# Kernel optimization log

Hardware: AMD Instinct MI355X
Metric: run time of the kernel (lower is better)

Reference implementation:

```python
import jax, jax.numpy as jnp
import numpy as np

N_NODES = 1_000_000
N_EDGES = 16_000_000
N_FEAT = 128
NUM_GRAPHS = 8192


def setup_inputs() -> dict:
    key = jax.random.key(0)
    k_x, k_e, k_b, k_w, k_pw, k_pb = jax.random.split(key, 6)
    x = jax.random.normal(k_x, (N_NODES, N_FEAT), dtype=jnp.float32)
    edge_index = jax.random.randint(k_e, (2, N_EDGES), 0, N_NODES, dtype=jnp.int64)
    batch = jnp.sort(jax.random.randint(k_b, (N_NODES,), 0, NUM_GRAPHS, dtype=jnp.int64))
    # GCNConv lin weight (F -> 1, no bias), xavier-ish scale
    W = jax.random.normal(k_w, (N_FEAT, 1), dtype=jnp.float32) * (6.0 / (N_FEAT + 1)) ** 0.5
    # post_pool Linear(1, 1, bias=True)
    pp_w = jax.random.normal(k_pw, (1, 1), dtype=jnp.float32)
    pp_b = jax.random.normal(k_pb, (1,), dtype=jnp.float32) * 0.1
    return {"x": x, "W": W, "pp_w": pp_w, "pp_b": pp_b,
            "edge_index": edge_index, "batch": batch}


def reference(x, W, pp_w, pp_b, edge_index, batch):
    N = x.shape[0]
    h = x @ W  # [N, 1] — tiny feature after GCNConv projection
    # add self-loops (PyG GCNConv default)
    loops = jnp.arange(N, dtype=edge_index.dtype)
    src = jnp.concatenate([edge_index[0], loops])  # message sources (col j)
    dst = jnp.concatenate([edge_index[1], loops])  # aggregation targets (row i)
    # symmetric degree normalization: deg over targets incl. self-loops
    deg = jax.ops.segment_sum(jnp.ones(src.shape[0], dtype=h.dtype), dst,
                              num_segments=N)
    dinv = jnp.where(deg > 0, jax.lax.rsqrt(deg), 0.0)
    norm = dinv[src] * dinv[dst]  # [E+N]
    # gather -> normalize -> scatter-add
    agg = jax.ops.segment_sum(norm[:, None] * h[src], dst, num_segments=N)  # [N,1]
    # global_add_pool by graph id
    pooled = jax.ops.segment_sum(agg, batch, num_segments=NUM_GRAPHS)  # [G,1]
    return pooled @ pp_w.T + pp_b  # Linear(1,1)
```

## Files before the change

kernel.cpp:

```cpp
#include <hip/hip_runtime.h>
#include <hip/hip_fp16.h>

#define NUM_GRAPHS 8192
#define BSHIFT 12
#define BSIZE 4096
#define CHUNK 8192

__global__ void __launch_bounds__(256)
pair_scatter_kernel(const int* __restrict__ src, const int* __restrict__ dst,
                    int E, int nchunks, int NBUK, int cap,
                    unsigned* __restrict__ cursor, unsigned* __restrict__ slab) {
    __shared__ unsigned cnt[256];
    __shared__ unsigned lbase[256];
    __shared__ unsigned sbase[256];
    __shared__ unsigned staged[CHUNK];
    __shared__ unsigned char sbuck[CHUNK];
    __shared__ unsigned s_tot;

    const int4* s4 = (const int4*)src;
    const int4* d4 = (const int4*)dst;
    int E4 = E >> 2;
    int tid = threadIdx.x;

    for (int chunk = blockIdx.x; chunk < nchunks; chunk += gridDim.x) {
        cnt[tid] = 0; __syncthreads();
        int b4 = chunk * (CHUNK / 4);
        int4 vd[8], vs[8];
        unsigned short r[32];
        #pragma unroll
        for (int k = 0; k < 8; ++k) {
            int idx = b4 + k * 256 + tid;
            if (idx < E4) { vd[k] = d4[idx]; vs[k] = s4[idx]; }
            else          { vd[k] = make_int4(-1, -1, -1, -1); }
        }
        #pragma unroll
        for (int k = 0; k < 8; ++k) {
            if (vd[k].x >= 0) {
                r[4*k+0] = (unsigned short)atomicAdd(&cnt[vd[k].x >> BSHIFT], 1u);
                r[4*k+1] = (unsigned short)atomicAdd(&cnt[vd[k].y >> BSHIFT], 1u);
                r[4*k+2] = (unsigned short)atomicAdd(&cnt[vd[k].z >> BSHIFT], 1u);
                r[4*k+3] = (unsigned short)atomicAdd(&cnt[vd[k].w >> BSHIFT], 1u);
            }
        }
        __syncthreads();
        lbase[tid] = cnt[tid]; __syncthreads();
        #pragma unroll
        for (int off = 1; off < 256; off <<= 1) {
            unsigned a = (tid >= off) ? lbase[tid - off] : 0u;
            __syncthreads();
            lbase[tid] += a;
            __syncthreads();
        }
        if (tid == 255) s_tot = lbase[255];
        if (tid < NBUK && cnt[tid]) sbase[tid] = atomicAdd(&cursor[tid], cnt[tid]);
        unsigned excl = lbase[tid] - cnt[tid];
        __syncthreads();
        lbase[tid] = excl;
        __syncthreads();

        #pragma unroll
        for (int k = 0; k < 8; ++k) {
            if (vd[k].x >= 0) {
                int d0 = vd[k].x, d1 = vd[k].y, d2 = vd[k].z, d3 = vd[k].w;
                unsigned b0 = (unsigned)d0 >> BSHIFT, b1 = (unsigned)d1 >> BSHIFT;
                unsigned b2 = (unsigned)d2 >> BSHIFT, b3 = (unsigned)d3 >> BSHIFT;
                unsigned p0 = lbase[b0] + r[4*k+0];
                unsigned p1 = lbase[b1] + r[4*k+1];
                unsigned p2 = lbase[b2] + r[4*k+2];
                unsigned p3 = lbase[b3] + r[4*k+3];
                staged[p0] = ((unsigned)(d0 & (BSIZE - 1)) << 20) | (unsigned)vs[k].x;
                staged[p1] = ((unsigned)(d1 & (BSIZE - 1)) << 20) | (unsigned)vs[k].y;
                staged[p2] = ((unsigned)(d2 & (BSIZE - 1)) << 20) | (unsigned)vs[k].z;
                staged[p3] = ((unsigned)(d3 & (BSIZE - 1)) << 20) | (unsigned)vs[k].w;
                sbuck[p0] = (unsigned char)b0;
                sbuck[p1] = (unsigned char)b1;
                sbuck[p2] = (unsigned char)b2;
                sbuck[p3] = (unsigned char)b3;
            }
        }
        __syncthreads();

        unsigned tot = s_tot;
        for (unsigned pos = tid; pos < tot; pos += 256) {
            unsigned b = sbuck[pos];
            unsigned gp = sbase[b] + (pos - lbase[b]);
            if (gp < (unsigned)cap) slab[(size_t)b * cap + gp] = staged[pos];
        }
        __syncthreads();
    }
    if (blockIdx.x == 0 && tid < (E & 3)) {
        int i = (E & ~3) + tid;
        int d = dst[i];
        unsigned p = atomicAdd(&cursor[d >> BSHIFT], 1u);
        if (p < (unsigned)cap)
            slab[(size_t)(d >> BSHIFT) * cap + p] =
                ((unsigned)(d & (BSIZE - 1)) << 20) | (unsigned)src[i];
    }
}

__global__ void __launch_bounds__(1024)
slab_hist_kernel(const unsigned* __restrict__ slab, int cap,
                 const unsigned* __restrict__ cursor,
                 unsigned* __restrict__ deg, int N) {
    __shared__ unsigned hist[BSIZE];
    int b = blockIdx.x, tid = threadIdx.x;
    unsigned n = cursor[b]; if (n > (unsigned)cap) n = cap;
    for (int t = tid; t < BSIZE; t += 1024) hist[t] = 0;
    __syncthreads();
    const unsigned* s = slab + (size_t)b * cap;
    for (unsigned i = tid; i < n; i += 1024) atomicAdd(&hist[s[i] >> 20], 1u);
    __syncthreads();
    int base = b << BSHIFT;
    int lim = N - base; if (lim > BSIZE) lim = BSIZE;
    for (int t = tid; t < lim; t += 1024) deg[base + t] = hist[t];
}

__global__ void node_kernel(const float* __restrict__ x,
                            const float* __restrict__ W,
                            const unsigned* __restrict__ deg,
                            const int* __restrict__ batch,
                            unsigned short* __restrict__ hsh,
                            unsigned* __restrict__ pkw, int N) {
    int gtid = blockIdx.x * blockDim.x + threadIdx.x;
    int wave = gtid >> 6;
    int lane = threadIdx.x & 63;
    int half = lane >> 5;
    int l32  = lane & 31;
    int node = wave * 2 + half;
    if (node >= N) return;

    const float4* xr = (const float4*)(x + (size_t)node * 128);
    float4 xv = xr[l32];
    float4 wv = ((const float4*)W)[l32];
    float v = xv.x * wv.x + xv.y * wv.y + xv.z * wv.z + xv.w * wv.w;
    #pragma unroll
    for (int d = 16; d >= 1; d >>= 1) v += __shfl_xor(v, d);

    if (l32 == 0) {
        float di = rsqrtf((float)(deg[node] + 1u));
        hsh[node] = __half_as_ushort(__float2half(di * v));
        pkw[node] = ((unsigned)batch[node] << 16) | __half_as_ushort(__float2half(di));
    }
}

__global__ void __launch_bounds__(1024)
aggregate_kernel(const unsigned* __restrict__ slab, int cap,
                 const unsigned* __restrict__ cursor,
                 const unsigned* __restrict__ pkw,
                 const unsigned short* __restrict__ hsh,
                 float* __restrict__ pooled, int N) {
    __shared__ float pool[NUM_GRAPHS];
    __shared__ unsigned pkw_s[BSIZE];
    int b = blockIdx.x, tid = threadIdx.x;
    int base = b << BSHIFT;
    int lim = N - base; if (lim > BSIZE) lim = BSIZE;

    for (int t = tid; t < NUM_GRAPHS; t += 1024) pool[t] = 0.0f;
    for (int t = tid; t < BSIZE; t += 1024) pkw_s[t] = (t < lim) ? pkw[base + t] : 0u;
    __syncthreads();

    for (int t = tid; t < lim; t += 1024) {
        unsigned w = pkw_s[t];
        float di = __half2float(__ushort_as_half((unsigned short)(w & 0xFFFFu)));
        float c = di * __half2float(__ushort_as_half(hsh[base + t]));
        atomicAdd(&pool[w >> 16], c);
    }

    unsigned n = cursor[b]; if (n > (unsigned)cap) n = cap;
    const unsigned* s = slab + (size_t)b * cap;
    for (unsigned i = tid; i < n; i += 1024) {
        unsigned e = s[i];
        unsigned w = pkw_s[e >> 20];
        float hv = __half2float(__ushort_as_half(hsh[e & 0xFFFFFu]));
        float di = __half2float(__ushort_as_half((unsigned short)(w & 0xFFFFu)));
        atomicAdd(&pool[w >> 16], hv * di);
    }
    __syncthreads();

    int g_lo = (int)(pkw_s[0] >> 16);
    int g_hi = (lim > 0) ? (int)(pkw_s[lim - 1] >> 16) : g_lo;
    for (int g = g_lo + tid; g <= g_hi; g += 1024) atomicAdd(&pooled[g], pool[g]);
}

__global__ void out_kernel(const float* __restrict__ pooled,
                           const float* __restrict__ pp_w,
                           const float* __restrict__ pp_b,
                           float* __restrict__ out) {
    int g = blockIdx.x * blockDim.x + threadIdx.x;
    if (g < NUM_GRAPHS) out[g] = pooled[g] * pp_w[0] + pp_b[0];
}

__global__ void deg_atomic_kernel(const int* __restrict__ dst, int E,
                                  unsigned* __restrict__ deg) {
    int tid = blockIdx.x * blockDim.x + threadIdx.x;
    int stride = gridDim.x * blockDim.x;
    for (int i = tid; i < E; i += stride) atomicAdd(&deg[dst[i]], 1u);
}

__global__ void pool_self_fb_kernel(const unsigned short* __restrict__ hsh,
                                    const unsigned* __restrict__ pkw,
                                    float* __restrict__ pooled, int N) {
    int i = blockIdx.x * blockDim.x + threadIdx.x;
    if (i >= N) return;
    unsigned w = pkw[i];
    float di = __half2float(__ushort_as_half((unsigned short)(w & 0xFFFFu)));
    atomicAdd(&pooled[w >> 16], di * __half2float(__ushort_as_half(hsh[i])));
}

__global__ void __launch_bounds__(512)
edge_direct_kernel(const int* __restrict__ src, const int* __restrict__ dst, int E,
                   const unsigned short* __restrict__ hsh,
                   const unsigned* __restrict__ pkw,
                   float* __restrict__ pooled) {
    __shared__ float pool[NUM_GRAPHS];
    for (int g = threadIdx.x; g < NUM_GRAPHS; g += 512) pool[g] = 0.0f;
    __syncthreads();
    int tid = blockIdx.x * 512 + threadIdx.x;
    int stride = gridDim.x * 512;
    for (int i = tid; i < E; i += stride) {
        unsigned w = pkw[dst[i]];
        float c = __half2float(__ushort_as_half(hsh[src[i]])) *
                  __half2float(__ushort_as_half((unsigned short)(w & 0xFFFFu)));
        atomicAdd(&pool[w >> 16], c);
    }
    __syncthreads();
    for (int g = threadIdx.x; g < NUM_GRAPHS; g += 512)
        if (pool[g] != 0.0f) atomicAdd(&pooled[g], pool[g]);
}

extern "C" void kernel_launch(void* const* d_in, const int* in_sizes, int n_in,
                              void* d_out, int out_size, void* d_ws, size_t ws_size,
                              hipStream_t stream) {
    const float* x    = (const float*)d_in[0];
    const float* W    = (const float*)d_in[1];
    const float* pp_w = (const float*)d_in[2];
    const float* pp_b = (const float*)d_in[3];
    const int*   ei   = (const int*)d_in[4];
    const int*   batch= (const int*)d_in[5];
    float* out = (float*)d_out;

    const int E = in_sizes[4] / 2;
    const int N = in_sizes[5];
    const int* src = ei;
    const int* dst = ei + E;
    int NBUK = (N + BSIZE - 1) >> BSHIFT;

    char* ws = (char*)d_ws;
    size_t off = 0;
    auto alloc = [&](size_t bytes) {
        size_t o = off; off = (off + bytes + 255) & ~(size_t)255; return o;
    };
    size_t deg_off    = alloc((size_t)N * 4);
    size_t hsh_off    = alloc((size_t)N * 2);
    size_t pkw_off    = alloc((size_t)N * 4);
    size_t pooled_off = alloc((size_t)NUM_GRAPHS * 4);
    size_t cursor_off = alloc(1024);

    int cap = E / NBUK + E / NBUK / 8 + 2048;
    size_t slab_off = alloc((size_t)NBUK * (size_t)cap * 4);

    bool slab_ok = (NBUK <= 256) && (N <= (1 << 20)) && (off <= ws_size);

    unsigned*       deg    = (unsigned*)(ws + deg_off);
    unsigned short* hsh    = (unsigned short*)(ws + hsh_off);
    unsigned*       pkw    = (unsigned*)(ws + pkw_off);
    float*          pooled = (float*)(ws + pooled_off);
    unsigned*       cursor = (unsigned*)(ws + cursor_off);
    unsigned*       slab   = (unsigned*)(ws + slab_off);

    hipMemsetAsync(pooled, 0, (size_t)NUM_GRAPHS * 4, stream);

    if (slab_ok) {
        hipMemsetAsync(cursor, 0, 1024, stream);
        int E4 = E >> 2;
        int nchunks = (E4 + (CHUNK / 4 - 1)) / (CHUNK / 4);
        int grid = nchunks < 2048 ? nchunks : 2048;
        pair_scatter_kernel<<<grid, 256, 0, stream>>>(src, dst, E, nchunks, NBUK,
                                                      cap, cursor, slab);
        slab_hist_kernel<<<NBUK, 1024, 0, stream>>>(slab, cap, cursor, deg, N);

        int node_blocks = (N + 7) / 8;
        node_kernel<<<node_blocks, 256, 0, stream>>>(x, W, deg, batch, hsh, pkw, N);

        aggregate_kernel<<<NBUK, 1024, 0, stream>>>(slab, cap, cursor, pkw, hsh,
                                                    pooled, N);
    } else {
        hipMemsetAsync(deg, 0, (size_t)N * 4, stream);
        deg_atomic_kernel<<<2048, 256, 0, stream>>>(dst, E, deg);
        int node_blocks = (N + 7) / 8;
        node_kernel<<<node_blocks, 256, 0, stream>>>(x, W, deg, batch, hsh, pkw, N);
        pool_self_fb_kernel<<<(N + 255) / 256, 256, 0, stream>>>(hsh, pkw, pooled, N);
        edge_direct_kernel<<<512, 512, 0, stream>>>(src, dst, E, hsh, pkw, pooled);
    }

    out_kernel<<<(NUM_GRAPHS + 255) / 256, 256, 0, stream>>>(pooled, pp_w, pp_b, out);
}
```

Before: 325.9 us.

## Run x@W projection concurrently with edge scatter via heterogeneous block roles

The edge bucket-scatter kernel and the node projection (x@W) now share one launch. One in three blocks does the scatter and the other two compute h, so the bandwidth-heavy 512MB read of x overlaps with the edge pass. The deg-to-normalisation step moves into the histogram kernel, which writes hsh/pkw directly and removes the separate node kernel and the deg buffer round trip. This adds an fp32 h buffer and makes the scatter's grid size fixed, so the two roles can contend for bandwidth and finish unevenly.

```diff
diff --git a/kernel.cpp b/kernel.cpp
--- a/kernel.cpp
+++ b/kernel.cpp
@@ -5,11 +5,15 @@
 #define BSHIFT 12
 #define BSIZE 4096
 #define CHUNK 8192
+#define SBLOCKS 1024
+#define HBLOCKS 2048
 
 __global__ void __launch_bounds__(256)
-pair_scatter_kernel(const int* __restrict__ src, const int* __restrict__ dst,
-                    int E, int nchunks, int NBUK, int cap,
-                    unsigned* __restrict__ cursor, unsigned* __restrict__ slab) {
+fused_scatter_h_kernel(const int* __restrict__ src, const int* __restrict__ dst,
+                       int E, int nchunks, int NBUK, int cap,
+                       unsigned* __restrict__ cursor, unsigned* __restrict__ slab,
+                       const float* __restrict__ x, const float* __restrict__ W,
+                       float* __restrict__ h, int N) {
     __shared__ unsigned cnt[256];
     __shared__ unsigned lbase[256];
     __shared__ unsigned sbase[256];
@@ -17,91 +21,115 @@
     __shared__ unsigned char sbuck[CHUNK];
     __shared__ unsigned s_tot;
 
-    const int4* s4 = (const int4*)src;
-    const int4* d4 = (const int4*)dst;
-    int E4 = E >> 2;
+    int bid = blockIdx.x;
+    int rem = bid % 3;
+    int grp = bid / 3;
     int tid = threadIdx.x;
 
-    for (int chunk = blockIdx.x; chunk < nchunks; chunk += gridDim.x) {
-        cnt[tid] = 0; __syncthreads();
-        int b4 = chunk * (CHUNK / 4);
-        int4 vd[8], vs[8];
-        unsigned short r[32];
-        #pragma unroll
-        for (int k = 0; k < 8; ++k) {
-            int idx = b4 + k * 256 + tid;
-            if (idx < E4) { vd[k] = d4[idx]; vs[k] = s4[idx]; }
-            else          { vd[k] = make_int4(-1, -1, -1, -1); }
+    if (rem == 0) {
+        const int4* s4 = (const int4*)src;
+        const int4* d4 = (const int4*)dst;
+        int E4 = E >> 2;
+        for (int chunk = grp; chunk < nchunks; chunk += SBLOCKS) {
+            cnt[tid] = 0; __syncthreads();
+            int b4 = chunk * (CHUNK / 4);
+            int4 vd[8], vs[8];
+            unsigned short r[32];
+            #pragma unroll
+            for (int k = 0; k < 8; ++k) {
+                int idx = b4 + k * 256 + tid;
+                if (idx < E4) { vd[k] = d4[idx]; vs[k] = s4[idx]; }
+                else          { vd[k] = make_int4(-1, -1, -1, -1); }
+            }
+            #pragma unroll
+            for (int k = 0; k < 8; ++k) {
+                if (vd[k].x >= 0) {
+                    r[4*k+0] = (unsigned short)atomicAdd(&cnt[vd[k].x >> BSHIFT], 1u);
+                    r[4*k+1] = (unsigned short)atomicAdd(&cnt[vd[k].y >> BSHIFT], 1u);
+                    r[4*k+2] = (unsigned short)atomicAdd(&cnt[vd[k].z >> BSHIFT], 1u);
+                    r[4*k+3] = (unsigned short)atomicAdd(&cnt[vd[k].w >> BSHIFT], 1u);
+                }
+            }
+            __syncthreads();
+            lbase[tid] = cnt[tid]; __syncthreads();
+            #pragma unroll
+            for (int off = 1; off < 256; off <<= 1) {
+                unsigned a = (tid >= off) ? lbase[tid - off] : 0u;
+                __syncthreads();
+                lbase[tid] += a;
+                __syncthreads();
+            }
+            if (tid == 255) s_tot = lbase[255];
+            if (tid < NBUK && cnt[tid]) sbase[tid] = atomicAdd(&cursor[tid], cnt[tid]);
+            unsigned excl = lbase[tid] - cnt[tid];
+            __syncthreads();
+            lbase[tid] = excl;
+            __syncthreads();
+
+            #pragma unroll
+            for (int k = 0; k < 8; ++k) {
+                if (vd[k].x >= 0) {
+                    int d0 = vd[k].x, d1 = vd[k].y, d2 = vd[k].z, d3 = vd[k].w;
+                    unsigned b0 = (unsigned)d0 >> BSHIFT, b1 = (unsigned)d1 >> BSHIFT;
+                    unsigned b2 = (unsigned)d2 >> BSHIFT, b3 = (unsigned)d3 >> BSHIFT;
+                    unsigned p0 = lbase[b0] + r[4*k+0];
+                    unsigned p1 = lbase[b1] + r[4*k+1];
+                    unsigned p2 = lbase[b2] + r[4*k+2];
+                    unsigned p3 = lbase[b3] + r[4*k+3];
+                    staged[p0] = ((unsigned)(d0 & (BSIZE - 1)) << 20) | (unsigned)vs[k].x;
+                    staged[p1] = ((unsigned)(d1 & (BSIZE - 1)) << 20) | (unsigned)vs[k].y;
+                    staged[p2] = ((unsigned)(d2 & (BSIZE - 1)) << 20) | (unsigned)vs[k].z;
+                    staged[p3] = ((unsigned)(d3 & (BSIZE - 1)) << 20) | (unsigned)vs[k].w;
+                    sbuck[p0] = (unsigned char)b0;
+                    sbuck[p1] = (unsigned char)b1;
+                    sbuck[p2] = (unsigned char)b2;
+                    sbuck[p3] = (unsigned char)b3;
+                }
+            }
+            __syncthreads();
+
+            unsigned tot = s_tot;
+            for (unsigned pos = tid; pos < tot; pos += 256) {
+                unsigned b = sbuck[pos];
+                unsigned gp = sbase[b] + (pos - lbase[b]);
+                if (gp < (unsigned)cap) slab[(size_t)b * cap + gp] = staged[pos];
+            }
+            __syncthreads();
         }
-        #pragma unroll
-        for (int k = 0; k < 8; ++k) {
-            if (vd[k].x >= 0) {
-                r[4*k+0] = (unsigned short)atomicAdd(&cnt[vd[k].x >> BSHIFT], 1u);
-                r[4*k+1] = (unsigned short)atomicAdd(&cnt[vd[k].y >> BSHIFT], 1u);
-                r[4*k+2] = (unsigned short)atomicAdd(&cnt[vd[k].z >> BSHIFT], 1u);
-                r[4*k+3] = (unsigned short)atomicAdd(&cnt[vd[k].w >> BSHIFT], 1u);
-            }
+        if (grp == 0 && tid < (E & 3)) {
+            int i = (E & ~3) + tid;
+            int d = dst[i];
+            unsigned p = atomicAdd(&cursor[d >> BSHIFT], 1u);
+            if (p < (unsigned)cap)
+                slab[(size_t)(d >> BSHIFT) * cap + p] =
+                    ((unsigned)(d & (BSIZE - 1)) << 20) | (unsigned)src[i];
         }
-        __syncthreads();
-        lbase[tid] = cnt[tid]; __syncthreads();
-        #pragma unroll
-        for (int off = 1; off < 256; off <<= 1) {
-            unsigned a = (tid >= off) ? lbase[tid - off] : 0u;
-            __syncthreads();
-            lbase[tid] += a;
-            __syncthreads();
+    } else {
+        int hid = grp * 2 + (rem - 1);
+        int wave = tid >> 6;
+        int lane = tid & 63;
+        int half = lane >> 5;
+        int l32  = lane & 31;
+        float4 wv = ((const float4*)W)[l32];
+        for (int base = hid * 8; base < N; base += HBLOCKS * 8) {
+            int node = base + wave * 2 + half;
+            if (node < N) {
+                float4 xv = ((const float4*)(x + (size_t)node * 128))[l32];
+                float v = xv.x * wv.x + xv.y * wv.y + xv.z * wv.z + xv.w * wv.w;
+                #pragma unroll
+                for (int d = 16; d >= 1; d >>= 1) v += __shfl_xor(v, d);
+                if (l32 == 0) h[node] = v;
+            }
         }
-        if (tid == 255) s_tot = lbase[255];
-        if (tid < NBUK && cnt[tid]) sbase[tid] = atomicAdd(&cursor[tid], cnt[tid]);
-        unsigned excl = lbase[tid] - cnt[tid];
-        __syncthreads();
-        lbase[tid] = excl;
-        __syncthreads();
-
-        #pragma unroll
-        for (int k = 0; k < 8; ++k) {
-            if (vd[k].x >= 0) {
-                int d0 = vd[k].x, d1 = vd[k].y, d2 = vd[k].z, d3 = vd[k].w;
-                unsigned b0 = (unsigned)d0 >> BSHIFT, b1 = (unsigned)d1 >> BSHIFT;
-                unsigned b2 = (unsigned)d2 >> BSHIFT, b3 = (unsigned)d3 >> BSHIFT;
-                unsigned p0 = lbase[b0] + r[4*k+0];
-                unsigned p1 = lbase[b1] + r[4*k+1];
-                unsigned p2 = lbase[b2] + r[4*k+2];
-                unsigned p3 = lbase[b3] + r[4*k+3];
-                staged[p0] = ((unsigned)(d0 & (BSIZE - 1)) << 20) | (unsigned)vs[k].x;
-                staged[p1] = ((unsigned)(d1 & (BSIZE - 1)) << 20) | (unsigned)vs[k].y;
-                staged[p2] = ((unsigned)(d2 & (BSIZE - 1)) << 20) | (unsigned)vs[k].z;
-                staged[p3] = ((unsigned)(d3 & (BSIZE - 1)) << 20) | (unsigned)vs[k].w;
-                sbuck[p0] = (unsigned char)b0;
-                sbuck[p1] = (unsigned char)b1;
-                sbuck[p2] = (unsigned char)b2;
-                sbuck[p3] = (unsigned char)b3;
-            }
-        }
-        __syncthreads();
-
-        unsigned tot = s_tot;
-        for (unsigned pos = tid; pos < tot; pos += 256) {
-            unsigned b = sbuck[pos];
-            unsigned gp = sbase[b] + (pos - lbase[b]);
-            if (gp < (unsigned)cap) slab[(size_t)b * cap + gp] = staged[pos];
-        }
-        __syncthreads();
-    }
-    if (blockIdx.x == 0 && tid < (E & 3)) {
-        int i = (E & ~3) + tid;
-        int d = dst[i];
-        unsigned p = atomicAdd(&cursor[d >> BSHIFT], 1u);
-        if (p < (unsigned)cap)
-            slab[(size_t)(d >> BSHIFT) * cap + p] =
-                ((unsigned)(d & (BSIZE - 1)) << 20) | (unsigned)src[i];
     }
 }
 
 __global__ void __launch_bounds__(1024)
-slab_hist_kernel(const unsigned* __restrict__ slab, int cap,
-                 const unsigned* __restrict__ cursor,
-                 unsigned* __restrict__ deg, int N) {
+hist_finalize_kernel(const unsigned* __restrict__ slab, int cap,
+                     const unsigned* __restrict__ cursor,
+                     const float* __restrict__ h, const int* __restrict__ batch,
+                     unsigned short* __restrict__ hsh, unsigned* __restrict__ pkw,
+                     int N) {
     __shared__ unsigned hist[BSIZE];
     int b = blockIdx.x, tid = threadIdx.x;
     unsigned n = cursor[b]; if (n > (unsigned)cap) n = cap;
@@ -112,34 +140,11 @@
     __syncthreads();
     int base = b << BSHIFT;
     int lim = N - base; if (lim > BSIZE) lim = BSIZE;
-    for (int t = tid; t < lim; t += 1024) deg[base + t] = hist[t];
-}
-
-__global__ void node_kernel(const float* __restrict__ x,
-                            const float* __restrict__ W,
-                            const unsigned* __restrict__ deg,
-                            const int* __restrict__ batch,
-                            unsigned short* __restrict__ hsh,
-                            unsigned* __restrict__ pkw, int N) {
-    int gtid = blockIdx.x * blockDim.x + threadIdx.x;
-    int wave = gtid >> 6;
-    int lane = threadIdx.x & 63;
-    int half = lane >> 5;
-    int l32  = lane & 31;
-    int node = wave * 2 + half;
-    if (node >= N) return;
-
-    const float4* xr = (const float4*)(x + (size_t)node * 128);
-    float4 xv = xr[l32];
-    float4 wv = ((const float4*)W)[l32];
-    float v = xv.x * wv.x + xv.y * wv.y + xv.z * wv.z + xv.w * wv.w;
-    #pragma unroll
-    for (int d = 16; d >= 1; d >>= 1) v += __shfl_xor(v, d);
-
-    if (l32 == 0) {
-        float di = rsqrtf((float)(deg[node] + 1u));
-        hsh[node] = __half_as_ushort(__float2half(di * v));
-        pkw[node] = ((unsigned)batch[node] << 16) | __half_as_ushort(__float2half(di));
+    for (int t = tid; t < lim; t += 1024) {
+        float di = rsqrtf((float)(hist[t] + 1u));
+        hsh[base + t] = __half_as_ushort(__float2half(di * h[base + t]));
+        pkw[base + t] = ((unsigned)batch[base + t] << 16) |
+                        __half_as_ushort(__float2half(di));
     }
 }
 
@@ -197,6 +202,32 @@
     for (int i = tid; i < E; i += stride) atomicAdd(&deg[dst[i]], 1u);
 }
 
+__global__ void node_fb_kernel(const float* __restrict__ x,
+                               const float* __restrict__ W,
+                               const unsigned* __restrict__ deg,
+                               const int* __restrict__ batch,
+                               unsigned short* __restrict__ hsh,
+                               unsigned* __restrict__ pkw, int N) {
+    int gtid = blockIdx.x * blockDim.x + threadIdx.x;
+    int wave = gtid >> 6;
+    int lane = threadIdx.x & 63;
+    int half = lane >> 5;
+    int l32  = lane & 31;
+    int node = wave * 2 + half;
+    if (node >= N) return;
+    const float4* xr = (const float4*)(x + (size_t)node * 128);
+    float4 xv = xr[l32];
+    float4 wv = ((const float4*)W)[l32];
+    float v = xv.x * wv.x + xv.y * wv.y + xv.z * wv.z + xv.w * wv.w;
+    #pragma unroll
+    for (int d = 16; d >= 1; d >>= 1) v += __shfl_xor(v, d);
+    if (l32 == 0) {
+        float di = rsqrtf((float)(deg[node] + 1u));
+        hsh[node] = __half_as_ushort(__float2half(di * v));
+        pkw[node] = ((unsigned)batch[node] << 16) | __half_as_ushort(__float2half(di));
+    }
+}
+
 __global__ void pool_self_fb_kernel(const unsigned short* __restrict__ hsh,
                                     const unsigned* __restrict__ pkw,
                                     float* __restrict__ pooled, int N) {
@@ -251,6 +282,7 @@
         size_t o = off; off = (off + bytes + 255) & ~(size_t)255; return o;
     };
     size_t deg_off    = alloc((size_t)N * 4);
+    size_t h_off      = alloc((size_t)N * 4);
     size_t hsh_off    = alloc((size_t)N * 2);
     size_t pkw_off    = alloc((size_t)N * 4);
     size_t pooled_off = alloc((size_t)NUM_GRAPHS * 4);
@@ -262,6 +294,7 @@
     bool slab_ok = (NBUK <= 256) && (N <= (1 << 20)) && (off <= ws_size);
 
     unsigned*       deg    = (unsigned*)(ws + deg_off);
+    float*          h      = (float*)(ws + h_off);
     unsigned short* hsh    = (unsigned short*)(ws + hsh_off);
     unsigned*       pkw    = (unsigned*)(ws + pkw_off);
     float*          pooled = (float*)(ws + pooled_off);
@@ -274,21 +307,17 @@
         hipMemsetAsync(cursor, 0, 1024, stream);
         int E4 = E >> 2;
         int nchunks = (E4 + (CHUNK / 4 - 1)) / (CHUNK / 4);
-        int grid = nchunks < 2048 ? nchunks : 2048;
-        pair_scatter_kernel<<<grid, 256, 0, stream>>>(src, dst, E, nchunks, NBUK,
-                                                      cap, cursor, slab);
-        slab_hist_kernel<<<NBUK, 1024, 0, stream>>>(slab, cap, cursor, deg, N);
-
-        int node_blocks = (N + 7) / 8;
-        node_kernel<<<node_blocks, 256, 0, stream>>>(x, W, deg, batch, hsh, pkw, N);
-
+        fused_scatter_h_kernel<<<SBLOCKS + HBLOCKS, 256, 0, stream>>>(
+            src, dst, E, nchunks, NBUK, cap, cursor, slab, x, W, h, N);
+        hist_finalize_kernel<<<NBUK, 1024, 0, stream>>>(slab, cap, cursor, h,
+                                                        batch, hsh, pkw, N);
         aggregate_kernel<<<NBUK, 1024, 0, stream>>>(slab, cap, cursor, pkw, hsh,
                                                     pooled, N);
     } else {
         hipMemsetAsync(deg, 0, (size_t)N * 4, stream);
         deg_atomic_kernel<<<2048, 256, 0, stream>>>(dst, E, deg);
         int node_blocks = (N + 7) / 8;
-        node_kernel<<<node_blocks, 256, 0, stream>>>(x, W, deg, batch, hsh, pkw, N);
+        node_fb_kernel<<<node_blocks, 256, 0, stream>>>(x, W, deg, batch, hsh, pkw, N);
         pool_self_fb_kernel<<<(N + 255) / 256, 256, 0, stream>>>(hsh, pkw, pooled, N);
         edge_direct_kernel<<<512, 512, 0, stream>>>(src, dst, E, hsh, pkw, pooled);
     }
```

New measurement: 357.8 us. 9.8% more time.
